# Kernel tuning notes

Hardware: AMD Instinct MI355X
Metric: run time of the kernel (lower is better)

Reference implementation:

```python
import jax, jax.numpy as jnp
import numpy as np

NEG_SLOPE = 0.2


def gat_layer(x, src, dst, W, att_src, att_dst, bias, n_nodes):
    # PyG GATConv (heads=1): h = x @ W; per-edge logit = LeakyReLU(a_src.h[src] + a_dst.h[dst]);
    # softmax over edges grouped by destination node; out[d] = sum alpha * h[src] + bias.
    h = x @ W                                  # [N, F]
    a_s = h @ att_src                          # [N]
    a_d = h @ att_dst                          # [N]
    e = a_s[src] + a_d[dst]                    # [E]
    e = jnp.where(e > 0, e, NEG_SLOPE * e)     # leaky_relu
    m = jax.ops.segment_max(e, dst, num_segments=n_nodes)   # [N]
    w = jnp.exp(e - m[dst])                    # [E]
    z = jax.ops.segment_sum(w, dst, num_segments=n_nodes)   # [N]
    alpha = w / z[dst]                         # [E] (self-loops guarantee z>0)
    out = jax.ops.segment_sum(alpha[:, None] * h[src], dst, num_segments=n_nodes)
    return out + bias


def setup_inputs() -> dict:
    key = jax.random.key(0)
    ks = jax.random.split(key, 10)
    N, E, C_IN, H1, H2 = 100000, 3200000, 128, 50, 40
    x = jax.random.normal(ks[0], (N, C_IN), dtype=jnp.float32)
    edge_index = jax.random.randint(ks[1], (2, E), 0, N, dtype=jnp.int64)
    g1 = 1.0 / np.sqrt(C_IN)
    g2 = 1.0 / np.sqrt(H1)
    return {
        "x": x,
        "edge_index": edge_index,
        "W1": jax.random.normal(ks[2], (C_IN, H1), dtype=jnp.float32) * g1,
        "att_src1": jax.random.normal(ks[3], (H1,), dtype=jnp.float32) * g2,
        "att_dst1": jax.random.normal(ks[4], (H1,), dtype=jnp.float32) * g2,
        "bias1": jnp.zeros((H1,), dtype=jnp.float32),
        "W2": jax.random.normal(ks[5], (H1, H2), dtype=jnp.float32) * g2,
        "att_src2": jax.random.normal(ks[6], (H2,), dtype=jnp.float32) / np.sqrt(H2),
        "att_dst2": jax.random.normal(ks[7], (H2,), dtype=jnp.float32) / np.sqrt(H2),
        "bias2": jnp.zeros((H2,), dtype=jnp.float32),
    }


def reference(x, edge_index, W1, att_src1, att_dst1, bias1, W2, att_src2, att_dst2, bias2):
    n_nodes = x.shape[0]
    # PyG GATConv default add_self_loops=True: append (i, i) for every node.
    loop = jnp.arange(n_nodes, dtype=edge_index.dtype)
    src = jnp.concatenate([edge_index[0], loop])
    dst = jnp.concatenate([edge_index[1], loop])
    h = jax.nn.relu(gat_layer(x, src, dst, W1, att_src1, att_dst1, bias1, n_nodes))
    h = jax.nn.relu(gat_layer(h, src, dst, W2, att_src2, att_dst2, bias2, n_nodes))
    return h, edge_index
```

## Files before the change

### kernel.cpp

```cpp
#include <hip/hip_runtime.h>
#include <hip/hip_bf16.h>
#include <math.h>

#define NEG_SLOPE 0.2f
#define RBITS 8
#define RNODES 256
#define CHUNK 8192
#define CAP   9216
#define HS    32


__device__ __forceinline__ float waveReduceSum(float v) {
    #pragma unroll
    for (int off = 32; off > 0; off >>= 1) v += __shfl_xor(v, off);
    return v;
}

__device__ __forceinline__ unsigned pack_bf16(float a, float b) {
    __hip_bfloat162 p(__float2bfloat16(a), __float2bfloat16(b));
    return *reinterpret_cast<unsigned*>(&p);
}
__device__ __forceinline__ float bf16lo_f(unsigned u) { return __uint_as_float(u << 16); }
__device__ __forceinline__ float bf16hi_f(unsigned u) { return __uint_as_float(u & 0xFFFF0000u); }


__global__ void prep(const float* __restrict__ W1, float* __restrict__ WT1,
                     const float* __restrict__ W2, float* __restrict__ WT2,
                     int* __restrict__ bcursor,
                     int K1, int F1, int KP1, int FP1,
                     int K2, int F2, int KP2, int FP2, int NB) {
    int i = blockIdx.x * blockDim.x + threadIdx.x;
    int z1 = FP1 * KP1, z2 = FP2 * KP2;
    if (i < z1) {
        int f = i / KP1, k = i - f * KP1;
        WT1[i] = (f < F1 && k < K1) ? W1[k * F1 + f] : 0.f;
    } else if (i < z1 + z2) {
        int j = i - z1;
        int f = j / KP2, k = j - f * KP2;
        WT2[j] = (f < F2 && k < K2) ? W2[k * F2 + f] : 0.f;
    } else if (i < z1 + z2 + NB) {
        bcursor[i - z1 - z2] = 0;
    }
}


__global__ __launch_bounds__(512) void binning(
        const int* __restrict__ src, const int* __restrict__ dst,
        int* __restrict__ bcursor, int* __restrict__ binned,
        long E, int N, long TOT) {
    __shared__ int hist[512];
    __shared__ int base[512];
    int t = threadIdx.x;
    hist[t] = 0;
    __syncthreads();
    long c0 = blockIdx.x * (long)CHUNK;
    long c1 = c0 + CHUNK; if (c1 > TOT) c1 = TOT;
    for (long i = c0 + t; i < c1; i += 512) {
        int d = (i < E) ? dst[i] : (int)(i - E);
        atomicAdd(&hist[d >> RBITS], 1);
    }
    __syncthreads();
    {
        int c = hist[t];
        base[t] = c ? atomicAdd(&bcursor[t], c) : 0;
        hist[t] = 0;
    }
    __syncthreads();
    for (long i = c0 + t; i < c1; i += 512) {
        int s, d;
        if (i < E) { s = src[i]; d = dst[i]; } else { s = d = (int)(i - E); }
        int b = d >> RBITS;
        int p = base[b] + atomicAdd(&hist[b], 1);
        if (p >= CAP) p = CAP - 1;
        binned[(long)b * CAP + p] = ((d & (RNODES - 1)) << 17) | s;
    }
}

__global__ __launch_bounds__(512) void bucket_scan(
        const int* __restrict__ bcursor, int* __restrict__ bstarts,
        int* __restrict__ starts, int NB, int N, int TOT) {
    __shared__ int s[512];
    int t = threadIdx.x;
    int v = (t < NB) ? bcursor[t] : 0;
    s[t] = v;
    __syncthreads();
    for (int off = 1; off < 512; off <<= 1) {
        int u = (t >= off) ? s[t - off] : 0;
        __syncthreads();
        s[t] += u;
        __syncthreads();
    }
    int excl = s[t] - v;
    if (t < NB) bstarts[t] = excl;
    if (t == 0) { bstarts[NB] = TOT; starts[N] = TOT; }
}

__global__ __launch_bounds__(512) void bucket_csr(
        const int* __restrict__ binned, const int* __restrict__ bstarts,
        int* __restrict__ starts, int* __restrict__ csr_src, int N) {
    __shared__ int cnt[RNODES];
    __shared__ int scn[RNODES];
    int b = blockIdx.x, t = threadIdx.x;
    int node0 = b << RBITS;
    int R = N - node0; if (R > RNODES) R = RNODES;
    int e0 = bstarts[b];
    int ecnt = bstarts[b + 1] - e0;
    const int* bin = binned + (long)b * CAP;
    if (t < RNODES) cnt[t] = 0;
    __syncthreads();
    for (int i = t; i < ecnt; i += 512)
        atomicAdd(&cnt[bin[i] >> 17], 1);
    __syncthreads();
    int v = (t < RNODES) ? cnt[t] : 0;
    if (t < RNODES) scn[t] = v;
    __syncthreads();
    for (int off = 1; off < RNODES; off <<= 1) {
        int u = (t >= off && t < RNODES) ? scn[t - off] : 0;
        __syncthreads();
        if (t < RNODES) scn[t] += u;
        __syncthreads();
    }
    if (t < RNODES) {
        int excl = scn[t] - v;
        if (t < R) starts[node0 + t] = e0 + excl;
        cnt[t] = excl;
    }
    __syncthreads();
    for (int i = t; i < ecnt; i += 512) {
        int packed = bin[i];
        int ld = packed >> 17;
        int p = atomicAdd(&cnt[ld], 1);
        csr_src[e0 + p] = packed & 0x1FFFF;
    }
}

template <int K, int KP, int F, int FPH>
__global__ __launch_bounds__(512) void gemm_tile(
        const float* __restrict__ x, const float* __restrict__ WT,
        const float* __restrict__ att_s, const float* __restrict__ att_d,
        unsigned* __restrict__ hb, float* __restrict__ as_, float* __restrict__ ad_,
        int N) {
    __shared__ float xT[KP * 65];
    __shared__ float asl[64], adl[64];
    int t = threadIdx.x;
    int lane = t & 63;
    int w = t >> 6;
    long n0 = (long)blockIdx.x * 64;
    int n = (int)n0 + lane;

    if (t < 64) { asl[t] = 0.f; adl[t] = 0.f; }
    for (int idx = t; idx < KP * 64; idx += 512) {
        int nn = idx / KP, k = idx - nn * KP;
        float v = 0.f;
        if (k < K && n0 + nn < N) v = x[(n0 + nn) * (long)K + k];
        xT[k * 65 + nn] = v;
    }
    __syncthreads();

    int f0 = __builtin_amdgcn_readfirstlane(w * 8);
    float acc[8] = {0.f, 0.f, 0.f, 0.f, 0.f, 0.f, 0.f, 0.f};
    if (f0 < F) {
        const float* wbase = WT + (long)f0 * KP;
        for (int k0 = 0; k0 < KP; k0 += 4) {
            float x0 = xT[(k0 + 0) * 65 + lane];
            float x1 = xT[(k0 + 1) * 65 + lane];
            float x2 = xT[(k0 + 2) * 65 + lane];
            float x3 = xT[(k0 + 3) * 65 + lane];
            #pragma unroll
            for (int j = 0; j < 8; ++j) {
                const float* wr = wbase + j * KP + k0;
                float a = acc[j];
                a = fmaf(wr[0], x0, a);
                a = fmaf(wr[1], x1, a);
                a = fmaf(wr[2], x2, a);
                a = fmaf(wr[3], x3, a);
                acc[j] = a;
            }
        }
        float ps = 0.f, pd = 0.f;
        #pragma unroll
        for (int j = 0; j < 8; ++j) {
            float sa = (f0 + j < F) ? att_s[f0 + j] : 0.f;
            float da = (f0 + j < F) ? att_d[f0 + j] : 0.f;
            ps = fmaf(acc[j], sa, ps);
            pd = fmaf(acc[j], da, pd);
        }
        atomicAdd(&asl[lane], ps);
        atomicAdd(&adl[lane], pd);
    }
    __syncthreads();

    if (f0 < F && n < N) {
        int f0h = f0 >> 1;
        #pragma unroll
        for (int q = 0; q < 4; ++q) {
            int fp = f0h + q;
            if (fp < FPH) hb[(long)n * HS + fp] = pack_bf16(acc[2 * q], acc[2 * q + 1]);
        }
    }
    if (w == 0 && n < N) { as_[n] = asl[lane]; ad_[n] = adl[lane]; }
}

template <int F>
__global__ __launch_bounds__(256) void gat_gather(
                           const int* __restrict__ csr_src, const int* __restrict__ starts,
                           const float* __restrict__ as_, const float* __restrict__ ad_,
                           const unsigned* __restrict__ hb, const float* __restrict__ bias,
                           float* __restrict__ out, int N) {
    constexpr int NU4 = (F + 7) / 8;
    int lane = threadIdx.x & 63;
    int g  = lane >> 3;
    int fl = lane & 7;
    bool actf = (fl < NU4);
    long wave = (blockIdx.x * (long)blockDim.x + threadIdx.x) >> 6;
    if (wave >= N) return;
    int d = (int)wave;
    int s0 = starts[d], s1 = starts[d + 1];
    float add = ad_[d];
    const unsigned* hbase = hb + 4 * fl;

    float lsum = 0.f;
    float a0 = 0.f, a1 = 0.f, a2 = 0.f, a3 = 0.f;
    float a4 = 0.f, a5 = 0.f, a6 = 0.f, a7 = 0.f;

    for (int base = s0; base < s1; base += 64) {
        int k = base + lane;
        int s = (k < s1) ? csr_src[k] : 0;
        unsigned soff = (unsigned)s << 5;
        float e = as_[s] + add;
        e = e > 0.f ? e : NEG_SLOPE * e;
        float w = (k < s1) ? __expf(e) : 0.f;
        lsum += w;
        int cnt = min(64, s1 - base);
        int nst = (cnt + 7) >> 3;
        int j = 0;
        for (; j + 4 <= nst; j += 4) {
            int i0 = 8 * j + g;
            unsigned so0 = __shfl(soff, i0);
            unsigned so1 = __shfl(soff, i0 + 8);
            unsigned so2 = __shfl(soff, i0 + 16);
            unsigned so3 = __shfl(soff, i0 + 24);
            uint4 h0 = make_uint4(0u,0u,0u,0u), h1 = h0, h2 = h0, h3 = h0;
            if (actf) {
                h0 = *(const uint4*)(hbase + so0);
                h1 = *(const uint4*)(hbase + so1);
                h2 = *(const uint4*)(hbase + so2);
                h3 = *(const uint4*)(hbase + so3);
            }
            float w0 = __shfl(w, i0);
            float w1 = __shfl(w, i0 + 8);
            float w2 = __shfl(w, i0 + 16);
            float w3 = __shfl(w, i0 + 24);
            a0 = fmaf(w0, bf16lo_f(h0.x), a0); a1 = fmaf(w0, bf16hi_f(h0.x), a1);
            a2 = fmaf(w0, bf16lo_f(h0.y), a2); a3 = fmaf(w0, bf16hi_f(h0.y), a3);
            a4 = fmaf(w0, bf16lo_f(h0.z), a4); a5 = fmaf(w0, bf16hi_f(h0.z), a5);
            a6 = fmaf(w0, bf16lo_f(h0.w), a6); a7 = fmaf(w0, bf16hi_f(h0.w), a7);
            a0 = fmaf(w1, bf16lo_f(h1.x), a0); a1 = fmaf(w1, bf16hi_f(h1.x), a1);
            a2 = fmaf(w1, bf16lo_f(h1.y), a2); a3 = fmaf(w1, bf16hi_f(h1.y), a3);
            a4 = fmaf(w1, bf16lo_f(h1.z), a4); a5 = fmaf(w1, bf16hi_f(h1.z), a5);
            a6 = fmaf(w1, bf16lo_f(h1.w), a6); a7 = fmaf(w1, bf16hi_f(h1.w), a7);
            a0 = fmaf(w2, bf16lo_f(h2.x), a0); a1 = fmaf(w2, bf16hi_f(h2.x), a1);
            a2 = fmaf(w2, bf16lo_f(h2.y), a2); a3 = fmaf(w2, bf16hi_f(h2.y), a3);
            a4 = fmaf(w2, bf16lo_f(h2.z), a4); a5 = fmaf(w2, bf16hi_f(h2.z), a5);
            a6 = fmaf(w2, bf16lo_f(h2.w), a6); a7 = fmaf(w2, bf16hi_f(h2.w), a7);
            a0 = fmaf(w3, bf16lo_f(h3.x), a0); a1 = fmaf(w3, bf16hi_f(h3.x), a1);
            a2 = fmaf(w3, bf16lo_f(h3.y), a2); a3 = fmaf(w3, bf16hi_f(h3.y), a3);
            a4 = fmaf(w3, bf16lo_f(h3.z), a4); a5 = fmaf(w3, bf16hi_f(h3.z), a5);
            a6 = fmaf(w3, bf16lo_f(h3.w), a6); a7 = fmaf(w3, bf16hi_f(h3.w), a7);
        }
        for (; j < nst; ++j) {
            int idx = 8 * j + g;
            float wp = __shfl(w, idx);
            unsigned so = __shfl(soff, idx);
            if (actf) {
                uint4 hv = *(const uint4*)(hbase + so);
                a0 = fmaf(wp, bf16lo_f(hv.x), a0); a1 = fmaf(wp, bf16hi_f(hv.x), a1);
                a2 = fmaf(wp, bf16lo_f(hv.y), a2); a3 = fmaf(wp, bf16hi_f(hv.y), a3);
                a4 = fmaf(wp, bf16lo_f(hv.z), a4); a5 = fmaf(wp, bf16hi_f(hv.z), a5);
                a6 = fmaf(wp, bf16lo_f(hv.w), a6); a7 = fmaf(wp, bf16hi_f(hv.w), a7);
            }
        }
    }

    #pragma unroll
    for (int off = 8; off < 64; off <<= 1) {
        a0 += __shfl_xor(a0, off); a1 += __shfl_xor(a1, off);
        a2 += __shfl_xor(a2, off); a3 += __shfl_xor(a3, off);
        a4 += __shfl_xor(a4, off); a5 += __shfl_xor(a5, off);
        a6 += __shfl_xor(a6, off); a7 += __shfl_xor(a7, off);
    }
    float l = waveReduceSum(lsum);

    if (actf) {
        float inv = 1.f / l;
        int fb = 8 * fl;
        float v[8] = {a0, a1, a2, a3, a4, a5, a6, a7};
        float2* orow = (float2*)(out + (long)d * F + fb);
        #pragma unroll
        for (int i = 0; i < 8; i += 2) {
            if (fb + i < F) {
                float u0 = v[i]     * inv + bias[fb + i];
                float u1 = v[i + 1] * inv + bias[fb + i + 1];
                u0 = u0 > 0.f ? u0 : 0.f;
                u1 = u1 > 0.f ? u1 : 0.f;
                orow[i >> 1] = make_float2(u0, u1);
            }
        }
    }
}

__global__ void copy_edges4(const int4* __restrict__ ei, float4* __restrict__ out, long n4) {
    long i = blockIdx.x * (long)blockDim.x + threadIdx.x;
    if (i < n4) {
        int4 v = ei[i];
        out[i] = make_float4((float)v.x, (float)v.y, (float)v.z, (float)v.w);
    }
}
__global__ void copy_edges_tail(const int* __restrict__ ei, float* __restrict__ out,
                                long lo, long n) {
    long i = lo + blockIdx.x * (long)blockDim.x + threadIdx.x;
    if (i < n) out[i] = (float)ei[i];
}


extern "C" void kernel_launch(void* const* d_in, const int* in_sizes, int n_in,
                              void* d_out, int out_size, void* d_ws, size_t ws_size,
                              hipStream_t stream) {
    const float* x         = (const float*)d_in[0];
    const int*   edge_idx  = (const int*)d_in[1];
    const float* W1        = (const float*)d_in[2];
    const float* att_src1  = (const float*)d_in[3];
    const float* att_dst1  = (const float*)d_in[4];
    const float* bias1     = (const float*)d_in[5];
    const float* W2        = (const float*)d_in[6];
    const float* att_src2  = (const float*)d_in[7];
    const float* att_dst2  = (const float*)d_in[8];
    const float* bias2     = (const float*)d_in[9];

    const int  CIN = 128, F1 = 50, F2 = 40;
    const int  KP1 = 128, FP1 = 56;
    const int  KP2 = 52,  FP2 = 40;
    const int  N = in_sizes[0] / CIN;
    const long E = in_sizes[1] / 2;
    const int* src = edge_idx;
    const int* dst = edge_idx + E;
    const long TOT = E + N;
    const int  NB = (N + RNODES - 1) >> RBITS;

    char* wsb = (char*)d_ws;
    size_t regionA = (size_t)NB * CAP * 4;
    if ((size_t)N * HS * 4 > regionA) regionA = (size_t)N * HS * 4;
    int*      binned = (int*)wsb;
    unsigned* hb     = (unsigned*)wsb;
    float*    hout   = (float*)(wsb + regionA);
    float*    as_    = hout + (long)N * F1;
    float*    ad_    = as_ + N;
    int*      starts  = (int*)(ad_ + N);
    int*      csr_src = starts + (N + 1);
    int*      bstarts = csr_src + TOT;
    int*      bcursor = bstarts + (NB + 1);
    float*    WT1     = (float*)(bcursor + NB + 3);
    float*    WT2     = WT1 + FP1 * KP1;

    float* out_h = (float*)d_out;
    float* out_e = out_h + (long)N * F2;

    const int B = 256;
    const int nodeWaveBlocks = (N + 3) / 4;
    const int nTileBlocks = (N + 63) / 64;
    const int nBinBlocks = (int)((TOT + CHUNK - 1) / CHUNK);
    const int prepElems = FP1 * KP1 + FP2 * KP2 + NB;

    prep<<<dim3((prepElems + B - 1) / B), dim3(B), 0, stream>>>(
        W1, WT1, W2, WT2, bcursor, CIN, F1, KP1, FP1, F1, F2, KP2, FP2, NB);
    binning<<<dim3(nBinBlocks), dim3(512), 0, stream>>>(src, dst, bcursor, binned, E, N, TOT);
    bucket_scan<<<dim3(1), dim3(512), 0, stream>>>(bcursor, bstarts, starts, NB, N, (int)TOT);
    bucket_csr<<<dim3(NB), dim3(512), 0, stream>>>(binned, bstarts, starts, csr_src, N);

    gemm_tile<CIN, KP1, F1, FP1 / 2><<<dim3(nTileBlocks), dim3(512), 0, stream>>>(x, WT1, att_src1, att_dst1, hb, as_, ad_, N);
    gat_gather<F1><<<dim3(nodeWaveBlocks), dim3(B), 0, stream>>>(csr_src, starts, as_, ad_, hb, bias1, hout, N);

    gemm_tile<F1, KP2, F2, FP2 / 2><<<dim3(nTileBlocks), dim3(512), 0, stream>>>(hout, WT2, att_src2, att_dst2, hb, as_, ad_, N);
    gat_gather<F2><<<dim3(nodeWaveBlocks), dim3(B), 0, stream>>>(csr_src, starts, as_, ad_, hb, bias2, out_h, N);

    long n_e = 2 * E;
    long n4  = n_e / 4;
    copy_edges4<<<dim3((int)((n4 + B - 1) / B)), dim3(B), 0, stream>>>((const int4*)edge_idx, (float4*)out_e, n4);
    if (n_e - n4 * 4 > 0)
        copy_edges_tail<<<dim3(1), dim3(B), 0, stream>>>(edge_idx, out_e, n4 * 4, n_e);
}
```

Baseline: 406.5 us.

## Use persistent waves with atomic work queue for GAT gather

Replaces the one-wave-per-node launch of the gather kernel with a fixed grid of 2048 blocks whose waves pull batches of 4 destination nodes from a global atomic counter. The counters are zeroed in the prep kernel alongside the bucket cursors. This aims to cut block launch and scheduling overhead and to balance the uneven per-node degree across waves. It adds one atomic per batch and serialises the nodes within each wave, which can reduce memory-level parallelism. Output stores are now limited to lanes with g==0 to avoid redundant writes.

```diff
diff --git a/kernel.cpp b/kernel.cpp
--- a/kernel.cpp
+++ b/kernel.cpp
@@ -8,6 +8,7 @@
 #define CHUNK 8192
 #define CAP   9216
 #define HS    32
+#define NBATCH 4
 
 
 __device__ __forceinline__ float waveReduceSum(float v) {
@@ -28,7 +29,7 @@
                      const float* __restrict__ W2, float* __restrict__ WT2,
                      int* __restrict__ bcursor,
                      int K1, int F1, int KP1, int FP1,
-                     int K2, int F2, int KP2, int FP2, int NB) {
+                     int K2, int F2, int KP2, int FP2, int NBZ) {
     int i = blockIdx.x * blockDim.x + threadIdx.x;
     int z1 = FP1 * KP1, z2 = FP2 * KP2;
     if (i < z1) {
@@ -38,7 +39,7 @@
         int j = i - z1;
         int f = j / KP2, k = j - f * KP2;
         WT2[j] = (f < F2 && k < K2) ? W2[k * F2 + f] : 0.f;
-    } else if (i < z1 + z2 + NB) {
+    } else if (i < z1 + z2 + NBZ) {
         bcursor[i - z1 - z2] = 0;
     }
 }
@@ -206,104 +207,113 @@
                            const int* __restrict__ csr_src, const int* __restrict__ starts,
                            const float* __restrict__ as_, const float* __restrict__ ad_,
                            const unsigned* __restrict__ hb, const float* __restrict__ bias,
-                           float* __restrict__ out, int N) {
+                           float* __restrict__ out, int N, int* __restrict__ qc) {
     constexpr int NU4 = (F + 7) / 8;
     int lane = threadIdx.x & 63;
     int g  = lane >> 3;
     int fl = lane & 7;
     bool actf = (fl < NU4);
-    long wave = (blockIdx.x * (long)blockDim.x + threadIdx.x) >> 6;
-    if (wave >= N) return;
-    int d = (int)wave;
-    int s0 = starts[d], s1 = starts[d + 1];
-    float add = ad_[d];
     const unsigned* hbase = hb + 4 * fl;
 
-    float lsum = 0.f;
-    float a0 = 0.f, a1 = 0.f, a2 = 0.f, a3 = 0.f;
-    float a4 = 0.f, a5 = 0.f, a6 = 0.f, a7 = 0.f;
-
-    for (int base = s0; base < s1; base += 64) {
-        int k = base + lane;
-        int s = (k < s1) ? csr_src[k] : 0;
-        unsigned soff = (unsigned)s << 5;
-        float e = as_[s] + add;
-        e = e > 0.f ? e : NEG_SLOPE * e;
-        float w = (k < s1) ? __expf(e) : 0.f;
-        lsum += w;
-        int cnt = min(64, s1 - base);
-        int nst = (cnt + 7) >> 3;
-        int j = 0;
-        for (; j + 4 <= nst; j += 4) {
-            int i0 = 8 * j + g;
-            unsigned so0 = __shfl(soff, i0);
-            unsigned so1 = __shfl(soff, i0 + 8);
-            unsigned so2 = __shfl(soff, i0 + 16);
-            unsigned so3 = __shfl(soff, i0 + 24);
-            uint4 h0 = make_uint4(0u,0u,0u,0u), h1 = h0, h2 = h0, h3 = h0;
-            if (actf) {
-                h0 = *(const uint4*)(hbase + so0);
-                h1 = *(const uint4*)(hbase + so1);
-                h2 = *(const uint4*)(hbase + so2);
-                h3 = *(const uint4*)(hbase + so3);
+    for (;;) {
+        int b;
+        if (lane == 0) b = atomicAdd(qc, 1);
+        b = __shfl(b, 0);
+        int nlo = b * NBATCH;
+        if (nlo >= N) break;
+        int nhi = nlo + NBATCH; if (nhi > N) nhi = N;
+
+        for (int d = nlo; d < nhi; ++d) {
+            int s0 = starts[d], s1 = starts[d + 1];
+            float add = ad_[d];
+
+            float lsum = 0.f;
+            float a0 = 0.f, a1 = 0.f, a2 = 0.f, a3 = 0.f;
+            float a4 = 0.f, a5 = 0.f, a6 = 0.f, a7 = 0.f;
+
+            for (int base = s0; base < s1; base += 64) {
+                int k = base + lane;
+                int s = (k < s1) ? csr_src[k] : 0;
+                unsigned soff = (unsigned)s * HS;
+                float e = as_[s] + add;
+                e = e > 0.f ? e : NEG_SLOPE * e;
+                float w = (k < s1) ? __expf(e) : 0.f;
+                lsum += w;
+                int cnt = min(64, s1 - base);
+                int nst = (cnt + 7) >> 3;
+                int j = 0;
+                for (; j + 4 <= nst; j += 4) {
+                    int i0 = 8 * j + g;
+                    unsigned so0 = __shfl(soff, i0);
+                    unsigned so1 = __shfl(soff, i0 + 8);
+                    unsigned so2 = __shfl(soff, i0 + 16);
+                    unsigned so3 = __shfl(soff, i0 + 24);
+                    uint4 h0 = make_uint4(0u,0u,0u,0u), h1 = h0, h2 = h0, h3 = h0;
+                    if (actf) {
+                        h0 = *(const uint4*)(hbase + so0);
+                        h1 = *(const uint4*)(hbase + so1);
+                        h2 = *(const uint4*)(hbase + so2);
+                        h3 = *(const uint4*)(hbase + so3);
+                    }
+                    float w0 = __shfl(w, i0);
+                    float w1 = __shfl(w, i0 + 8);
+                    float w2 = __shfl(w, i0 + 16);
+                    float w3 = __shfl(w, i0 + 24);
+                    a0 = fmaf(w0, bf16lo_f(h0.x), a0); a1 = fmaf(w0, bf16hi_f(h0.x), a1);
+                    a2 = fmaf(w0, bf16lo_f(h0.y), a2); a3 = fmaf(w0, bf16hi_f(h0.y), a3);
+                    a4 = fmaf(w0, bf16lo_f(h0.z), a4); a5 = fmaf(w0, bf16hi_f(h0.z), a5);
+                    a6 = fmaf(w0, bf16lo_f(h0.w), a6); a7 = fmaf(w0, bf16hi_f(h0.w), a7);
+                    a0 = fmaf(w1, bf16lo_f(h1.x), a0); a1 = fmaf(w1, bf16hi_f(h1.x), a1);
+                    a2 = fmaf(w1, bf16lo_f(h1.y), a2); a3 = fmaf(w1, bf16hi_f(h1.y), a3);
+                    a4 = fmaf(w1, bf16lo_f(h1.z), a4); a5 = fmaf(w1, bf16hi_f(h1.z), a5);
+                    a6 = fmaf(w1, bf16lo_f(h1.w), a6); a7 = fmaf(w1, bf16hi_f(h1.w), a7);
+                    a0 = fmaf(w2, bf16lo_f(h2.x), a0); a1 = fmaf(w2, bf16hi_f(h2.x), a1);
+                    a2 = fmaf(w2, bf16lo_f(h2.y), a2); a3 = fmaf(w2, bf16hi_f(h2.y), a3);
+                    a4 = fmaf(w2, bf16lo_f(h2.z), a4); a5 = fmaf(w2, bf16hi_f(h2.z), a5);
+                    a6 = fmaf(w2, bf16lo_f(h2.w), a6); a7 = fmaf(w2, bf16hi_f(h2.w), a7);
+                    a0 = fmaf(w3, bf16lo_f(h3.x), a0); a1 = fmaf(w3, bf16hi_f(h3.x), a1);
+                    a2 = fmaf(w3, bf16lo_f(h3.y), a2); a3 = fmaf(w3, bf16hi_f(h3.y), a3);
+                    a4 = fmaf(w3, bf16lo_f(h3.z), a4); a5 = fmaf(w3, bf16hi_f(h3.z), a5);
+                    a6 = fmaf(w3, bf16lo_f(h3.w), a6); a7 = fmaf(w3, bf16hi_f(h3.w), a7);
+                }
+                for (; j < nst; ++j) {
+                    int idx = 8 * j + g;
+                    float wp = __shfl(w, idx);
+                    unsigned so = __shfl(soff, idx);
+                    if (actf) {
+                        uint4 hv = *(const uint4*)(hbase + so);
+                        a0 = fmaf(wp, bf16lo_f(hv.x), a0); a1 = fmaf(wp, bf16hi_f(hv.x), a1);
+                        a2 = fmaf(wp, bf16lo_f(hv.y), a2); a3 = fmaf(wp, bf16hi_f(hv.y), a3);
+                        a4 = fmaf(wp, bf16lo_f(hv.z), a4); a5 = fmaf(wp, bf16hi_f(hv.z), a5);
+                        a6 = fmaf(wp, bf16lo_f(hv.w), a6); a7 = fmaf(wp, bf16hi_f(hv.w), a7);
+                    }
+                }
             }
-            float w0 = __shfl(w, i0);
-            float w1 = __shfl(w, i0 + 8);
-            float w2 = __shfl(w, i0 + 16);
-            float w3 = __shfl(w, i0 + 24);
-            a0 = fmaf(w0, bf16lo_f(h0.x), a0); a1 = fmaf(w0, bf16hi_f(h0.x), a1);
-            a2 = fmaf(w0, bf16lo_f(h0.y), a2); a3 = fmaf(w0, bf16hi_f(h0.y), a3);
-            a4 = fmaf(w0, bf16lo_f(h0.z), a4); a5 = fmaf(w0, bf16hi_f(h0.z), a5);
-            a6 = fmaf(w0, bf16lo_f(h0.w), a6); a7 = fmaf(w0, bf16hi_f(h0.w), a7);
-            a0 = fmaf(w1, bf16lo_f(h1.x), a0); a1 = fmaf(w1, bf16hi_f(h1.x), a1);
-            a2 = fmaf(w1, bf16lo_f(h1.y), a2); a3 = fmaf(w1, bf16hi_f(h1.y), a3);
-            a4 = fmaf(w1, bf16lo_f(h1.z), a4); a5 = fmaf(w1, bf16hi_f(h1.z), a5);
-            a6 = fmaf(w1, bf16lo_f(h1.w), a6); a7 = fmaf(w1, bf16hi_f(h1.w), a7);
-            a0 = fmaf(w2, bf16lo_f(h2.x), a0); a1 = fmaf(w2, bf16hi_f(h2.x), a1);
-            a2 = fmaf(w2, bf16lo_f(h2.y), a2); a3 = fmaf(w2, bf16hi_f(h2.y), a3);
-            a4 = fmaf(w2, bf16lo_f(h2.z), a4); a5 = fmaf(w2, bf16hi_f(h2.z), a5);
-            a6 = fmaf(w2, bf16lo_f(h2.w), a6); a7 = fmaf(w2, bf16hi_f(h2.w), a7);
-            a0 = fmaf(w3, bf16lo_f(h3.x), a0); a1 = fmaf(w3, bf16hi_f(h3.x), a1);
-            a2 = fmaf(w3, bf16lo_f(h3.y), a2); a3 = fmaf(w3, bf16hi_f(h3.y), a3);
-            a4 = fmaf(w3, bf16lo_f(h3.z), a4); a5 = fmaf(w3, bf16hi_f(h3.z), a5);
-            a6 = fmaf(w3, bf16lo_f(h3.w), a6); a7 = fmaf(w3, bf16hi_f(h3.w), a7);
-        }
-        for (; j < nst; ++j) {
-            int idx = 8 * j + g;
-            float wp = __shfl(w, idx);
-            unsigned so = __shfl(soff, idx);
-            if (actf) {
-                uint4 hv = *(const uint4*)(hbase + so);
-                a0 = fmaf(wp, bf16lo_f(hv.x), a0); a1 = fmaf(wp, bf16hi_f(hv.x), a1);
-                a2 = fmaf(wp, bf16lo_f(hv.y), a2); a3 = fmaf(wp, bf16hi_f(hv.y), a3);
-                a4 = fmaf(wp, bf16lo_f(hv.z), a4); a5 = fmaf(wp, bf16hi_f(hv.z), a5);
-                a6 = fmaf(wp, bf16lo_f(hv.w), a6); a7 = fmaf(wp, bf16hi_f(hv.w), a7);
+
+            #pragma unroll
+            for (int off = 8; off < 64; off <<= 1) {
+                a0 += __shfl_xor(a0, off); a1 += __shfl_xor(a1, off);
+                a2 += __shfl_xor(a2, off); a3 += __shfl_xor(a3, off);
+                a4 += __shfl_xor(a4, off); a5 += __shfl_xor(a5, off);
+                a6 += __shfl_xor(a6, off); a7 += __shfl_xor(a7, off);
             }
-        }
-    }
-
-    #pragma unroll
-    for (int off = 8; off < 64; off <<= 1) {
-        a0 += __shfl_xor(a0, off); a1 += __shfl_xor(a1, off);
-        a2 += __shfl_xor(a2, off); a3 += __shfl_xor(a3, off);
-        a4 += __shfl_xor(a4, off); a5 += __shfl_xor(a5, off);
-        a6 += __shfl_xor(a6, off); a7 += __shfl_xor(a7, off);
-    }
-    float l = waveReduceSum(lsum);
-
-    if (actf) {
-        float inv = 1.f / l;
-        int fb = 8 * fl;
-        float v[8] = {a0, a1, a2, a3, a4, a5, a6, a7};
-        float2* orow = (float2*)(out + (long)d * F + fb);
-        #pragma unroll
-        for (int i = 0; i < 8; i += 2) {
-            if (fb + i < F) {
-                float u0 = v[i]     * inv + bias[fb + i];
-                float u1 = v[i + 1] * inv + bias[fb + i + 1];
-                u0 = u0 > 0.f ? u0 : 0.f;
-                u1 = u1 > 0.f ? u1 : 0.f;
-                orow[i >> 1] = make_float2(u0, u1);
+            float l = waveReduceSum(lsum);
+
+            if (actf && g == 0) {
+                float inv = 1.f / l;
+                int fb = 8 * fl;
+                float v[8] = {a0, a1, a2, a3, a4, a5, a6, a7};
+                float2* orow = (float2*)(out + (long)d * F + fb);
+                #pragma unroll
+                for (int i = 0; i < 8; i += 2) {
+                    if (fb + i < F) {
+                        float u0 = v[i]     * inv + bias[fb + i];
+                        float u1 = v[i + 1] * inv + bias[fb + i + 1];
+                        u0 = u0 > 0.f ? u0 : 0.f;
+                        u1 = u1 > 0.f ? u1 : 0.f;
+                        orow[i >> 1] = make_float2(u0, u1);
+                    }
+                }
             }
         }
     }
@@ -359,6 +369,8 @@
     int*      csr_src = starts + (N + 1);
     int*      bstarts = csr_src + TOT;
     int*      bcursor = bstarts + (NB + 1);
+    int*      qc1     = bcursor + NB;
+    int*      qc2     = bcursor + NB + 1;
     float*    WT1     = (float*)(bcursor + NB + 3);
     float*    WT2     = WT1 + FP1 * KP1;
 
@@ -366,22 +378,26 @@
     float* out_e = out_h + (long)N * F2;
 
     const int B = 256;
-    const int nodeWaveBlocks = (N + 3) / 4;
+    const int gatBlocks = 2048;
     const int nTileBlocks = (N + 63) / 64;
     const int nBinBlocks = (int)((TOT + CHUNK - 1) / CHUNK);
-    const int prepElems = FP1 * KP1 + FP2 * KP2 + NB;
+    const int prepElems = FP1 * KP1 + FP2 * KP2 + NB + 2;
 
     prep<<<dim3((prepElems + B - 1) / B), dim3(B), 0, stream>>>(
-        W1, WT1, W2, WT2, bcursor, CIN, F1, KP1, FP1, F1, F2, KP2, FP2, NB);
+        W1, WT1, W2, WT2, bcursor, CIN, F1, KP1, FP1, F1, F2, KP2, FP2, NB + 2);
     binning<<<dim3(nBinBlocks), dim3(512), 0, stream>>>(src, dst, bcursor, binned, E, N, TOT);
     bucket_scan<<<dim3(1), dim3(512), 0, stream>>>(bcursor, bstarts, starts, NB, N, (int)TOT);
     bucket_csr<<<dim3(NB), dim3(512), 0, stream>>>(binned, bstarts, starts, csr_src, N);
 
-    gemm_tile<CIN, KP1, F1, FP1 / 2><<<dim3(nTileBlocks), dim3(512), 0, stream>>>(x, WT1, att_src1, att_dst1, hb, as_, ad_, N);
-    gat_gather<F1><<<dim3(nodeWaveBlocks), dim3(B), 0, stream>>>(csr_src, starts, as_, ad_, hb, bias1, hout, N);
-
-    gemm_tile<F1, KP2, F2, FP2 / 2><<<dim3(nTileBlocks), dim3(512), 0, stream>>>(hout, WT2, att_src2, att_dst2, hb, as_, ad_, N);
-    gat_gather<F2><<<dim3(nodeWaveBlocks), dim3(B), 0, stream>>>(csr_src, starts, as_, ad_, hb, bias2, out_h, N);
+    gemm_tile<CIN, KP1, F1, FP1 / 2><<<dim3(nTileBlocks), dim3(512), 0, stream>>>(
+        x, WT1, att_src1, att_dst1, hb, as_, ad_, N);
+    gat_gather<F1><<<dim3(gatBlocks), dim3(B), 0, stream>>>(
+        csr_src, starts, as_, ad_, hb, bias1, hout, N, qc1);
+
+    gemm_tile<F1, KP2, F2, FP2 / 2><<<dim3(nTileBlocks), dim3(512), 0, stream>>>(
+        hout, WT2, att_src2, att_dst2, hb, as_, ad_, N);
+    gat_gather<F2><<<dim3(gatBlocks), dim3(B), 0, stream>>>(
+        csr_src, starts, as_, ad_, hb, bias2, out_h, N, qc2);
 
     long n_e = 2 * E;
     long n4  = n_e / 4;
```

Result: slower. 1.081 ms (+165.9%).
